# Performance work log

Measured on AMD Instinct MI355X. Metric: run time of the kernel, lower is better.

The kernel has to match this reference:

```python
import jax, jax.numpy as jnp
import numpy as np

N = 1_500_000
NUM_VOXELS = 262_144  # static segment count (replaces torch.unique's dynamic voxel count)
VSIZE = np.array([0.32, 0.32, 0.32], np.float32)
PC_MIN = np.array([-74.88, -74.88, -2.0], np.float32)
GRID = np.array([468, 468, 32], np.int64)
BN_EPS = 1e-3


def setup_inputs() -> dict:
    rng = np.random.default_rng(0)
    # points uniformly inside the point-cloud range -> the range mask is all-true
    xyz = rng.uniform(PC_MIN, PC_MIN + VSIZE * GRID - 1e-3, size=(N, 3)).astype(np.float32)
    feats = rng.uniform(0.0, 1.0, size=(N, 1)).astype(np.float32)
    coords = np.floor((xyz - PC_MIN) / VSIZE).astype(np.int64)
    merge = coords[:, 0] * (GRID[1] * GRID[2]) + coords[:, 1] * GRID[2] + coords[:, 2]
    unq_inv = (merge % NUM_VOXELS).astype(np.int32)  # static-size stand-in for unique inverse ids
    key = jax.random.key(0)
    k1, k2 = jax.random.split(key)
    return {
        'points_xyz': jnp.asarray(xyz),
        'point_feats': jnp.asarray(feats),
        'w1': jax.random.normal(k1, (11, 32), jnp.float32) * 0.1,
        'g1': jnp.ones((32,), jnp.float32),
        'b1': jnp.zeros((32,), jnp.float32),
        'w2': jax.random.normal(k2, (64, 64), jnp.float32) * 0.1,
        'g2': jnp.ones((64,), jnp.float32),
        'b2': jnp.zeros((64,), jnp.float32),
        'unq_inv': jnp.asarray(unq_inv),
    }


def _pfn(x, w, g, b, unq_inv):
    # Linear(bias=False) -> BatchNorm1d(train-mode batch stats, eps=1e-3) -> ReLU -> scatter_max
    y = x @ w
    mu = jnp.mean(y, axis=0)
    var = jnp.var(y, axis=0)
    y = (y - mu) * jax.lax.rsqrt(var + BN_EPS) * g + b
    y = jax.nn.relu(y)
    # relu output >= 0; clamp empty segments (-inf) to 0, matching torch_scatter's zero fill
    y_max = jnp.maximum(jax.ops.segment_max(y, unq_inv, num_segments=NUM_VOXELS), 0.0)
    return y, y_max


def reference(points_xyz, point_feats, w1, g1, b1, w2, g2, b2, unq_inv):
    vsize = jnp.asarray(VSIZE)
    pc_min = jnp.asarray(PC_MIN)
    coords = jnp.floor((points_xyz - pc_min) / vsize)  # [N,3] float voxel coords

    # scatter_mean of xyz per voxel -> cluster-relative offsets
    ones = jnp.ones((points_xyz.shape[0],), points_xyz.dtype)
    cnt = jax.ops.segment_sum(ones, unq_inv, num_segments=NUM_VOXELS)
    vsum = jax.ops.segment_sum(points_xyz, unq_inv, num_segments=NUM_VOXELS)
    vmean = vsum / jnp.maximum(cnt, 1.0)[:, None]
    f_cluster = points_xyz - vmean[unq_inv]

    # offset from voxel center
    f_center = points_xyz - (coords * vsize + vsize * 0.5 + pc_min)
    dist = jnp.linalg.norm(points_xyz, axis=1, keepdims=True)

    feat = jnp.concatenate([points_xyz, point_feats, f_cluster, f_center, dist], axis=-1)  # [N,11]

    x, x_max = _pfn(feat, w1, g1, b1, unq_inv)            # [N,32], [V,32]
    x = jnp.concatenate([x, x_max[unq_inv]], axis=1)       # [N,64]
    _, out = _pfn(x, w2, g2, b2, unq_inv)                  # [V,64] pillar features
    return out
```

## Files before the change

### kernel.cpp

```cpp
#include <hip/hip_runtime.h>

#define NPTS 1500000
#define NVOX 262144
#define BN_EPS 1e-3f
#define PAD 1500160
#define NB_PT 5860
#define NB_L2 11720

typedef __attribute__((ext_vector_type(8))) short bf16x8;
typedef __attribute__((ext_vector_type(4))) float f32x4;

__device__ __forceinline__ unsigned fkey(float f) {
    unsigned u = __float_as_uint(f);
    return u ^ ((unsigned)(((int)u) >> 31) | 0x80000000u);
}
__device__ __forceinline__ float funkey(unsigned k) {
    unsigned u = (k & 0x80000000u) ? (k ^ 0x80000000u) : ~k;
    return __uint_as_float(u);
}
#define KEY_NEG_INF 0x007FFFFFu

__device__ __forceinline__ float bf2f(unsigned short h) {
    union { unsigned u; float f; } x; x.u = ((unsigned)h) << 16; return x.f;
}
__device__ __forceinline__ unsigned short f2bf(float f) {
    union { float f; unsigned u; } x; x.f = f;
    unsigned r = x.u + 0x7FFFu + ((x.u >> 16) & 1u);
    return (unsigned short)(r >> 16);
}
__device__ __forceinline__ unsigned packbf(float a, float b) {
    return (unsigned)f2bf(a) | ((unsigned)f2bf(b) << 16);
}

__device__ __forceinline__ void make_feat(float x, float y, float z, float w,
                                          float mx, float my, float mz, float* f) {
    const float VS = 0.32f;
    const float PMX = -74.88f, PMY = -74.88f, PMZ = -2.0f;
    f[0] = x; f[1] = y; f[2] = z; f[3] = w;
    f[4] = x - mx; f[5] = y - my; f[6] = z - mz;
    float cx = floorf((x - PMX) / VS);
    float cy = floorf((y - PMY) / VS);
    float cz = floorf((z - PMZ) / VS);
    f[7] = x - (cx * VS + 0.5f * VS + PMX);
    f[8] = y - (cy * VS + 0.5f * VS + PMY);
    f[9] = z - (cz * VS + 0.5f * VS + PMZ);
    f[10] = sqrtf(x * x + y * y + z * z);
}

__global__ void k_init(unsigned* __restrict__ okeys, unsigned* __restrict__ xmraw,
                       int* __restrict__ cntv, float* __restrict__ zf,
                       int* __restrict__ svid, const float* __restrict__ w2,
                       uint4* __restrict__ wfrag) {
    long t0 = (long)blockIdx.x * 256 + threadIdx.x;
    long st = (long)gridDim.x * 256;
    uint4 kneg = make_uint4(KEY_NEG_INF, KEY_NEG_INF, KEY_NEG_INF, KEY_NEG_INF);
    for (long i = t0; i < (long)NVOX * 16; i += st) ((uint4*)okeys)[i] = kneg;
    for (long i = t0; i < (long)NVOX * 8; i += st) ((uint4*)xmraw)[i] = kneg;
    for (long i = t0; i < NVOX / 4; i += st) ((int4*)cntv)[i] = make_int4(0, 0, 0, 0);
    for (long i = t0; i < (1024 + 256 * 64 + 256 * 128) / 4; i += st)
        ((float4*)zf)[i] = make_float4(0.f, 0.f, 0.f, 0.f);
    if (t0 < PAD - NPTS) svid[NPTS + t0] = -1;
    if (blockIdx.x == 0 && threadIdx.x < 64) {
        int l = threadIdx.x;
        int lr = l & 15, lk = l >> 4;
        #pragma unroll
        for (int nt = 0; nt < 4; ++nt)
            #pragma unroll
            for (int kt = 0; kt < 2; ++kt) {
                int col = nt * 16 + lr;
                int kb = kt * 32 + lk * 8;
                unsigned u[4];
                #pragma unroll
                for (int j = 0; j < 4; ++j) {
                    float a = w2[(kb + 2 * j) * 64 + col];
                    float b = w2[(kb + 2 * j + 1) * 64 + col];
                    u[j] = packbf(a, b);
                }
                wfrag[(nt * 2 + kt) * 64 + l] = make_uint4(u[0], u[1], u[2], u[3]);
            }
    }
}

__global__ void k_hist(const int* __restrict__ unq, int* __restrict__ cntv) {
    int i = blockIdx.x * blockDim.x + threadIdx.x;
    if (i < NPTS) atomicAdd(&cntv[unq[i]], 1);
}

__global__ void k_scanA(const int* __restrict__ cntv, int* __restrict__ startv,
                        int* __restrict__ bsum) {
    __shared__ int lds[256];
    int t = threadIdx.x;
    int idx4 = blockIdx.x * 256 + t;
    int4 cv = ((const int4*)cntv)[idx4];
    int s0 = cv.x, s1 = s0 + cv.y, s2 = s1 + cv.z, T = s2 + cv.w;
    lds[t] = T;
    __syncthreads();
    for (int o = 1; o < 256; o <<= 1) {
        int v = (t >= o) ? lds[t - o] : 0;
        __syncthreads();
        lds[t] += v;
        __syncthreads();
    }
    int excl = lds[t] - T;
    int4 ov; ov.x = excl; ov.y = excl + s0; ov.z = excl + s1; ov.w = excl + s2;
    ((int4*)startv)[idx4] = ov;
    if (t == 255) bsum[blockIdx.x] = lds[255];
}

__global__ void k_scanC(int* __restrict__ startv, int* __restrict__ offv,
                        const int* __restrict__ bsum) {
    __shared__ int lds[256];
    int t = threadIdx.x;
    int b = bsum[t];
    lds[t] = b;
    __syncthreads();
    for (int o = 1; o < 256; o <<= 1) {
        int v = (t >= o) ? lds[t - o] : 0;
        __syncthreads();
        lds[t] += v;
        __syncthreads();
    }
    int add = (blockIdx.x > 0) ? lds[blockIdx.x - 1] : 0;
    int idx4 = blockIdx.x * 256 + t;
    int4 v = ((int4*)startv)[idx4];
    v.x += add; v.y += add; v.z += add; v.w += add;
    ((int4*)startv)[idx4] = v;
    ((int4*)offv)[idx4] = v;
}

__global__ void k_scatter2(const float* __restrict__ xyz, const float* __restrict__ pf,
                           const int* __restrict__ unq, int* __restrict__ offv,
                           float4* __restrict__ spts, int* __restrict__ svid) {
    int i = blockIdx.x * blockDim.x + threadIdx.x;
    if (i >= NPTS) return;
    int v = unq[i];
    int pos = atomicAdd(&offv[v], 1);
    float4 p;
    p.x = xyz[3 * i + 0]; p.y = xyz[3 * i + 1]; p.z = xyz[3 * i + 2]; p.w = pf[i];
    spts[pos] = p;
    svid[pos] = v;
}

__global__ void k_vmean2(const float4* __restrict__ spts, const int* __restrict__ cntv,
                         const int* __restrict__ startv, float4* __restrict__ vmeanv) {
    int v = blockIdx.x * 256 + threadIdx.x;
    int cnt = cntv[v];
    if (!cnt) return;
    int st = startv[v];
    float sx = 0, sy = 0, sz = 0;
    for (int j = 0; j < cnt; ++j) {
        float4 p = spts[st + j];
        sx += p.x; sy += p.y; sz += p.z;
    }
    float inv = 1.0f / (float)cnt;
    vmeanv[v] = make_float4(sx * inv, sy * inv, sz * inv, 0.f);
}

__device__ __forceinline__ void flush32(int v, float m, bool atom, int c,
                                        unsigned* __restrict__ xm) {
    if ((unsigned)v >= (unsigned)NVOX) return;
    if (atom) atomicMax(&xm[(size_t)v * 32 + c], fkey(m));
    else xm[(size_t)v * 32 + c] = fkey(m);
}
__device__ __forceinline__ void flush64(int v, float m, bool atom, int c,
                                        unsigned* __restrict__ ok) {
    if ((unsigned)v >= (unsigned)NVOX) return;
    if (atom) atomicMax(&ok[(size_t)v * 64 + c], fkey(m));
    else ok[(size_t)v * 64 + c] = fkey(m);
}

__global__ __launch_bounds__(256) void k_passA(
    const float4* __restrict__ spts, const int* __restrict__ svid,
    const float4* __restrict__ vmeanv, const float* __restrict__ w1,
    unsigned* __restrict__ xmraw, unsigned* __restrict__ y1bf,
    float* __restrict__ spart1) {
    __shared__ float ylds[4][32 * 33];
    int t = threadIdx.x;
    int lane = t & 63, wave = t >> 6;
    int rl = lane & 31, half = lane >> 5;
    long grow = (long)blockIdx.x * 128 + wave * 32 + rl;
    int vid = svid[grow];
    float yv[16];
    #pragma unroll
    for (int j = 0; j < 16; ++j) yv[j] = 0.f;
    if (vid >= 0) {
        float4 p = spts[grow];
        float4 vm = vmeanv[vid];
        float f[11];
        make_feat(p.x, p.y, p.z, p.w, vm.x, vm.y, vm.z, f);
        const float4* w1f = (const float4*)w1;
        #pragma unroll
        for (int k = 0; k < 11; ++k) {
            float fk = f[k];
            #pragma unroll
            for (int q = 0; q < 4; ++q) {
                float4 wq = w1f[k * 8 + half * 4 + q];
                yv[4 * q + 0] = fmaf(fk, wq.x, yv[4 * q + 0]);
                yv[4 * q + 1] = fmaf(fk, wq.y, yv[4 * q + 1]);
                yv[4 * q + 2] = fmaf(fk, wq.z, yv[4 * q + 2]);
                yv[4 * q + 3] = fmaf(fk, wq.w, yv[4 * q + 3]);
            }
        }
    }
    {
        unsigned ypk[8];
        #pragma unroll
        for (int q = 0; q < 8; ++q) ypk[q] = packbf(yv[2 * q], yv[2 * q + 1]);
        uint4* yb = (uint4*)y1bf;
        yb[grow * 4 + half * 2 + 0] = *(const uint4*)&ypk[0];
        yb[grow * 4 + half * 2 + 1] = *(const uint4*)&ypk[4];
    }
    float* yw = &ylds[wave][0];
    #pragma unroll
    for (int j = 0; j < 16; ++j) yw[rl * 33 + half * 16 + j] = yv[j];
    asm volatile("s_waitcnt lgkmcnt(0)" ::: "memory");
    __builtin_amdgcn_sched_barrier(0);
    int c = rl;
    int r0 = half * 16;
    float sa = 0.f, sq = 0.f;
    int cur_v = -2; float cur_m = 0.f; bool first = true;
    #pragma unroll
    for (int i = 0; i < 16; ++i) {
        int r = r0 + i;
        float y = yw[r * 33 + c];
        int v = __shfl(vid, r);
        sa += y; sq += y * y;
        if (i == 0) { cur_v = v; cur_m = y; }
        else if (v == cur_v) cur_m = fmaxf(cur_m, y);
        else {
            flush32(cur_v, cur_m, first, c, xmraw);
            first = false; cur_v = v; cur_m = y;
        }
    }
    flush32(cur_v, cur_m, true, c, xmraw);
    sa += __shfl_xor(sa, 32);
    sq += __shfl_xor(sq, 32);
    if (half == 0) {
        int slot = (blockIdx.x * 4 + wave) & 255;
        atomicAdd(&spart1[slot * 64 + c], sa);
        atomicAdd(&spart1[slot * 64 + 32 + c], sq);
    }
}

__global__ void k_fin1(const float* __restrict__ spart1, float* __restrict__ stats,
                       const float* __restrict__ g1, const float* __restrict__ b1) {
    __shared__ float cs[64];
    int t = threadIdx.x;
    float s = 0.f;
    for (int r = 0; r < 256; ++r) s += spart1[r * 64 + t];
    cs[t] = s;
    __syncthreads();
    if (t < 32) {
        float invn = 1.0f / (float)NPTS;
        float mu = cs[t] * invn;
        float var = cs[32 + t] * invn - mu * mu;
        float sc = rsqrtf(var + BN_EPS) * g1[t];
        stats[64 + t] = sc;
        stats[96 + t] = b1[t] - mu * sc;
    }
}

__global__ void k_xmz(const unsigned* __restrict__ xmraw,
                      const float* __restrict__ stats, unsigned* __restrict__ zxm) {
    int tid = blockIdx.x * 256 + threadIdx.x;
    int v = tid >> 2, q = tid & 3;
    uint4 a = ((const uint4*)xmraw)[v * 8 + q * 2];
    uint4 b = ((const uint4*)xmraw)[v * 8 + q * 2 + 1];
    float4 sc0 = ((const float4*)(stats + 64))[q * 2];
    float4 sh0 = ((const float4*)(stats + 96))[q * 2];
    float4 sc1 = ((const float4*)(stats + 64))[q * 2 + 1];
    float4 sh1 = ((const float4*)(stats + 96))[q * 2 + 1];
    uint4 o;
    o.x = packbf(fmaxf(0.f, fmaf(funkey(a.x), sc0.x, sh0.x)),
                 fmaxf(0.f, fmaf(funkey(a.y), sc0.y, sh0.y)));
    o.y = packbf(fmaxf(0.f, fmaf(funkey(a.z), sc0.z, sh0.z)),
                 fmaxf(0.f, fmaf(funkey(a.w), sc0.w, sh0.w)));
    o.z = packbf(fmaxf(0.f, fmaf(funkey(b.x), sc1.x, sh1.x)),
                 fmaxf(0.f, fmaf(funkey(b.y), sc1.y, sh1.y)));
    o.w = packbf(fmaxf(0.f, fmaf(funkey(b.z), sc1.z, sh1.z)),
                 fmaxf(0.f, fmaf(funkey(b.w), sc1.w, sh1.w)));
    ((uint4*)zxm)[v * 4 + q] = o;
}

__global__ __launch_bounds__(256) void k_l2(
    const int* __restrict__ svid, const unsigned* __restrict__ y1bf,
    const unsigned* __restrict__ zxm, const uint4* __restrict__ wfrag,
    const float* __restrict__ stats, float* __restrict__ spart2,
    unsigned* __restrict__ okeys) {
    __shared__ unsigned shbuf[4][1088];
    int t = threadIdx.x;
    int lane = t & 63, wave = t >> 6;
    int rl = lane & 31, half = lane >> 5;
    int lr = lane & 15, lk = lane >> 4;
    long brow = (long)blockIdx.x * 128 + wave * 32;
    int vid = svid[brow + rl];
    int vprev = __shfl(vid, (lane + 63) & 63);
    unsigned mask32 = (unsigned)(__ballot(rl > 0 && vid != vprev) & 0xFFFFFFFFull);

    uint4 bw[8];
    #pragma unroll
    for (int q = 0; q < 8; ++q) bw[q] = wfrag[q * 64 + lane];
    uint4 yu0 = ((const uint4*)y1bf)[(brow + rl) * 4 + half * 2];
    uint4 yu1 = ((const uint4*)y1bf)[(brow + rl) * 4 + half * 2 + 1];
    uint4 xa = make_uint4(0, 0, 0, 0), xb = make_uint4(0, 0, 0, 0);
    if (vid >= 0) {
        xa = ((const uint4*)zxm)[(size_t)vid * 4 + half * 2];
        xb = ((const uint4*)zxm)[(size_t)vid * 4 + half * 2 + 1];
    }

    unsigned zpk[8];
    if (vid >= 0) {
        unsigned yw[8] = {yu0.x, yu0.y, yu0.z, yu0.w, yu1.x, yu1.y, yu1.z, yu1.w};
        #pragma unroll
        for (int q = 0; q < 4; ++q) {
            float4 sc = ((const float4*)(stats + 64))[half * 4 + q];
            float4 sh = ((const float4*)(stats + 96))[half * 4 + q];
            float yA = bf2f((unsigned short)(yw[2 * q] & 0xFFFF));
            float yB = bf2f((unsigned short)(yw[2 * q] >> 16));
            float yC = bf2f((unsigned short)(yw[2 * q + 1] & 0xFFFF));
            float yD = bf2f((unsigned short)(yw[2 * q + 1] >> 16));
            zpk[2 * q + 0] = packbf(fmaxf(0.f, fmaf(yA, sc.x, sh.x)),
                                    fmaxf(0.f, fmaf(yB, sc.y, sh.y)));
            zpk[2 * q + 1] = packbf(fmaxf(0.f, fmaf(yC, sc.z, sh.z)),
                                    fmaxf(0.f, fmaf(yD, sc.w, sh.w)));
        }
    } else {
        #pragma unroll
        for (int q = 0; q < 8; ++q) zpk[q] = 0u;
    }
    {
        uint4* arow = (uint4*)&shbuf[wave][rl * 32];
        int sw = rl & 7;
        arow[(2 * half + 0) ^ sw] = *(const uint4*)&zpk[0];
        arow[(2 * half + 1) ^ sw] = *(const uint4*)&zpk[4];
        arow[(4 + 2 * half) ^ sw] = xa;
        arow[(5 + 2 * half) ^ sw] = xb;
    }
    asm volatile("s_waitcnt lgkmcnt(0)" ::: "memory");
    __builtin_amdgcn_sched_barrier(0);

    bf16x8 afr[2][2];
    #pragma unroll
    for (int mt = 0; mt < 2; ++mt)
        #pragma unroll
        for (int kt = 0; kt < 2; ++kt) {
            int riw = mt * 16 + lr;
            uint4 uu = ((const uint4*)&shbuf[wave][riw * 32])[(kt * 4 + lk) ^ (riw & 7)];
            afr[mt][kt] = __builtin_bit_cast(bf16x8, uu);
        }
    asm volatile("s_waitcnt lgkmcnt(0)" ::: "memory");
    __builtin_amdgcn_sched_barrier(0);

    f32x4 acc[2][4];
    #pragma unroll
    for (int mt = 0; mt < 2; ++mt)
        #pragma unroll
        for (int nt = 0; nt < 4; ++nt) {
            acc[mt][nt] = (f32x4){0.f, 0.f, 0.f, 0.f};
            #pragma unroll
            for (int kt = 0; kt < 2; ++kt)
                acc[mt][nt] = __builtin_amdgcn_mfma_f32_16x16x32_bf16(
                    afr[mt][kt], __builtin_bit_cast(bf16x8, bw[nt * 2 + kt]),
                    acc[mt][nt], 0, 0, 0);
        }

    unsigned* y2w = &shbuf[wave][0];
    #pragma unroll
    for (int mt = 0; mt < 2; ++mt)
        #pragma unroll
        for (int nt = 0; nt < 4; ++nt) {
            int col = nt * 16 + lr;
            int w0 = mt * 8 + lk * 2;
            y2w[col * 17 + w0] = packbf(acc[mt][nt][0], acc[mt][nt][1]);
            y2w[col * 17 + w0 + 1] = packbf(acc[mt][nt][2], acc[mt][nt][3]);
        }

    {
        float sa[4] = {0.f, 0.f, 0.f, 0.f}, sq[4] = {0.f, 0.f, 0.f, 0.f};
        #pragma unroll
        for (int mt = 0; mt < 2; ++mt)
            #pragma unroll
            for (int nt = 0; nt < 4; ++nt)
                #pragma unroll
                for (int e = 0; e < 4; ++e) {
                    float v = acc[mt][nt][e];
                    sa[nt] += v; sq[nt] += v * v;
                }
        #pragma unroll
        for (int nt = 0; nt < 4; ++nt) {
            sa[nt] += __shfl_xor(sa[nt], 16); sa[nt] += __shfl_xor(sa[nt], 32);
            sq[nt] += __shfl_xor(sq[nt], 16); sq[nt] += __shfl_xor(sq[nt], 32);
        }
        if (lk == 0) {
            int slot = (blockIdx.x * 4 + wave) & 255;
            #pragma unroll
            for (int nt = 0; nt < 4; ++nt) {
                atomicAdd(&spart2[slot * 128 + nt * 16 + lr], sa[nt]);
                atomicAdd(&spart2[slot * 128 + 64 + nt * 16 + lr], sq[nt]);
            }
        }
    }
    asm volatile("s_waitcnt lgkmcnt(0)" ::: "memory");
    __builtin_amdgcn_sched_barrier(0);

    {
        int c = lane;
        float cur_m = 0.f; bool first = true;
        #pragma unroll
        for (int q = 0; q < 16; ++q) {
            unsigned u = y2w[c * 17 + q];
            #pragma unroll
            for (int e = 0; e < 2; ++e) {
                int r = 2 * q + e;
                float d = bf2f((unsigned short)(e ? (u >> 16) : (u & 0xFFFF)));
                if (r == 0) cur_m = d;
                else if ((mask32 >> r) & 1u) {
                    int v = __shfl(vid, r - 1);
                    flush64(v, cur_m, first, c, okeys);
                    first = false; cur_m = d;
                } else cur_m = fmaxf(cur_m, d);
            }
        }
        int vlast = __shfl(vid, 31);
        flush64(vlast, cur_m, true, c, okeys);
    }
}

__global__ void k_fin2(const float* __restrict__ spart2, float* __restrict__ stats,
                       const float* __restrict__ g2, const float* __restrict__ b2) {
    __shared__ float cs[128];
    int t = threadIdx.x;
    float s = 0.f;
    for (int r = 0; r < 256; ++r) s += spart2[r * 128 + t];
    cs[t] = s;
    __syncthreads();
    if (t < 64) {
        float invn = 1.0f / (float)NPTS;
        float mu = cs[t] * invn;
        float var = cs[64 + t] * invn - mu * mu;
        float sc = rsqrtf(var + BN_EPS) * g2[t];
        stats[256 + t] = sc;
        stats[320 + t] = b2[t] - mu * sc;
    }
}

__global__ void k_out(unsigned* __restrict__ okeys, const float* __restrict__ stats) {
    int i4 = blockIdx.x * 256 + threadIdx.x;
    uint4 u = ((const uint4*)okeys)[i4];
    int c0 = (i4 & 15) * 4;
    float4 o;
    o.x = fmaxf(0.f, fmaf(funkey(u.x), stats[256 + c0 + 0], stats[320 + c0 + 0]));
    o.y = fmaxf(0.f, fmaf(funkey(u.y), stats[256 + c0 + 1], stats[320 + c0 + 1]));
    o.z = fmaxf(0.f, fmaf(funkey(u.z), stats[256 + c0 + 2], stats[320 + c0 + 2]));
    o.w = fmaxf(0.f, fmaf(funkey(u.w), stats[256 + c0 + 3], stats[320 + c0 + 3]));
    ((float4*)okeys)[i4] = o;
}

extern "C" void kernel_launch(void* const* d_in, const int* in_sizes, int n_in,
                              void* d_out, int out_size, void* d_ws, size_t ws_size,
                              hipStream_t stream) {
    const float* xyz = (const float*)d_in[0];
    const float* pf  = (const float*)d_in[1];
    const float* w1  = (const float*)d_in[2];
    const float* g1  = (const float*)d_in[3];
    const float* b1  = (const float*)d_in[4];
    const float* w2  = (const float*)d_in[5];
    const float* g2  = (const float*)d_in[6];
    const float* b2  = (const float*)d_in[7];
    const int*   unq = (const int*)d_in[8];

    float4* spts     = (float4*)d_ws;
    float4* vmeanv   = spts + PAD;
    int* svid        = (int*)(vmeanv + NVOX);
    unsigned* xmraw  = (unsigned*)(svid + PAD);
    int* cntv        = (int*)(xmraw + (size_t)NVOX * 32);
    int* startv      = cntv + NVOX;
    int* offv        = startv + NVOX;
    int* bsum        = offv + NVOX;
    float* stats     = (float*)(bsum + 256);
    float* spart1    = stats + 1024;
    float* spart2    = spart1 + 256 * 64;
    uint4* wfrag     = (uint4*)(spart2 + 256 * 128);
    unsigned* y1bf   = (unsigned*)(wfrag + 512);
    unsigned* zxm    = (unsigned*)spts;

    unsigned* okeys = (unsigned*)d_out;

    k_init<<<2048, 256, 0, stream>>>(okeys, xmraw, cntv, stats, svid, w2, wfrag);
    k_hist<<<NB_PT, 256, 0, stream>>>(unq, cntv);
    k_scanA<<<256, 256, 0, stream>>>(cntv, startv, bsum);
    k_scanC<<<256, 256, 0, stream>>>(startv, offv, bsum);
    k_scatter2<<<NB_PT, 256, 0, stream>>>(xyz, pf, unq, offv, spts, svid);
    k_vmean2<<<NVOX / 256, 256, 0, stream>>>(spts, cntv, startv, vmeanv);
    k_passA<<<NB_L2, 256, 0, stream>>>(spts, svid, vmeanv, w1, xmraw, y1bf, spart1);
    k_fin1<<<1, 64, 0, stream>>>(spart1, stats, g1, b1);
    k_xmz<<<NVOX * 4 / 256, 256, 0, stream>>>(xmraw, stats, zxm);
    k_l2<<<NB_L2, 256, 0, stream>>>(svid, y1bf, zxm, wfrag, stats, spart2, okeys);
    k_fin2<<<1, 128, 0, stream>>>(spart2, stats, g2, b2);
    k_out<<<NVOX * 16 / 256, 256, 0, stream>>>(okeys, stats);
}
```

Before: 378.1 us.

## Replace per-voxel atomic scatter with two-level bucket scatter and local sort

Points are first scattered into 2048 coarse buckets of 128 voxels using one global atomic counter per bucket, written to a staging buffer that reuses the y1bf space. A per-bucket kernel then places points at their final voxel positions using LDS atomics. The aim is to make the global writes and atomics in the scatter more localized and coalesced. The cost is an extra pass over the staged data, and the bucket counters become heavily contended global atomics.

```diff
diff --git a/kernel.cpp b/kernel.cpp
--- a/kernel.cpp
+++ b/kernel.cpp
@@ -6,6 +6,7 @@
 #define PAD 1500160
 #define NB_PT 5860
 #define NB_L2 11720
+#define NBUK 2048
 
 typedef __attribute__((ext_vector_type(8))) short bf16x8;
 typedef __attribute__((ext_vector_type(4))) float f32x4;
@@ -107,7 +108,7 @@
     if (t == 255) bsum[blockIdx.x] = lds[255];
 }
 
-__global__ void k_scanC(int* __restrict__ startv, int* __restrict__ offv,
+__global__ void k_scanC(int* __restrict__ startv, int* __restrict__ bukcur,
                         const int* __restrict__ bsum) {
     __shared__ int lds[256];
     int t = threadIdx.x;
@@ -125,20 +126,42 @@
     int4 v = ((int4*)startv)[idx4];
     v.x += add; v.y += add; v.z += add; v.w += add;
     ((int4*)startv)[idx4] = v;
-    ((int4*)offv)[idx4] = v;
-}
-
-__global__ void k_scatter2(const float* __restrict__ xyz, const float* __restrict__ pf,
-                           const int* __restrict__ unq, int* __restrict__ offv,
-                           float4* __restrict__ spts, int* __restrict__ svid) {
+    int vox0 = idx4 * 4;
+    if ((vox0 & 127) == 0) bukcur[vox0 >> 7] = v.x;
+}
+
+__global__ void k_bscat(const float* __restrict__ xyz, const float* __restrict__ pf,
+                        const int* __restrict__ unq, int* __restrict__ bukcur,
+                        float4* __restrict__ stage_p, int* __restrict__ stage_v) {
     int i = blockIdx.x * blockDim.x + threadIdx.x;
     if (i >= NPTS) return;
     int v = unq[i];
-    int pos = atomicAdd(&offv[v], 1);
+    int pos = atomicAdd(&bukcur[v >> 7], 1);
     float4 p;
     p.x = xyz[3 * i + 0]; p.y = xyz[3 * i + 1]; p.z = xyz[3 * i + 2]; p.w = pf[i];
-    spts[pos] = p;
-    svid[pos] = v;
+    stage_p[pos] = p;
+    stage_v[pos] = v;
+}
+
+__global__ __launch_bounds__(256) void k_bsort(
+    const float4* __restrict__ stage_p, const int* __restrict__ stage_v,
+    const int* __restrict__ startv, float4* __restrict__ spts,
+    int* __restrict__ svid) {
+    __shared__ int cnt[128];
+    int t = threadIdx.x;
+    if (t < 128) cnt[t] = 0;
+    __syncthreads();
+    int b = blockIdx.x;
+    int bstart = startv[b << 7];
+    int bend = (b == NBUK - 1) ? NPTS : startv[(b + 1) << 7];
+    for (int j = bstart + t; j < bend; j += 256) {
+        float4 p = stage_p[j];
+        int v = stage_v[j];
+        int lr = atomicAdd(&cnt[v & 127], 1);
+        int pos = startv[v] + lr;
+        spts[pos] = p;
+        svid[pos] = v;
+    }
 }
 
 __global__ void k_vmean2(const float4* __restrict__ spts, const int* __restrict__ cntv,
@@ -475,13 +498,15 @@
     unsigned* xmraw  = (unsigned*)(svid + PAD);
     int* cntv        = (int*)(xmraw + (size_t)NVOX * 32);
     int* startv      = cntv + NVOX;
-    int* offv        = startv + NVOX;
-    int* bsum        = offv + NVOX;
+    int* bukcur      = startv + NVOX;
+    int* bsum        = bukcur + NVOX;
     float* stats     = (float*)(bsum + 256);
     float* spart1    = stats + 1024;
     float* spart2    = spart1 + 256 * 64;
     uint4* wfrag     = (uint4*)(spart2 + 256 * 128);
     unsigned* y1bf   = (unsigned*)(wfrag + 512);
+    float4* stage_p  = (float4*)y1bf;
+    int* stage_v     = (int*)(stage_p + PAD);
     unsigned* zxm    = (unsigned*)spts;
 
     unsigned* okeys = (unsigned*)d_out;
@@ -489,8 +514,9 @@
     k_init<<<2048, 256, 0, stream>>>(okeys, xmraw, cntv, stats, svid, w2, wfrag);
     k_hist<<<NB_PT, 256, 0, stream>>>(unq, cntv);
     k_scanA<<<256, 256, 0, stream>>>(cntv, startv, bsum);
-    k_scanC<<<256, 256, 0, stream>>>(startv, offv, bsum);
-    k_scatter2<<<NB_PT, 256, 0, stream>>>(xyz, pf, unq, offv, spts, svid);
+    k_scanC<<<256, 256, 0, stream>>>(startv, bukcur, bsum);
+    k_bscat<<<NB_PT, 256, 0, stream>>>(xyz, pf, unq, bukcur, stage_p, stage_v);
+    k_bsort<<<NBUK, 256, 0, stream>>>(stage_p, stage_v, startv, spts, svid);
     k_vmean2<<<NVOX / 256, 256, 0, stream>>>(spts, cntv, startv, vmeanv);
     k_passA<<<NB_L2, 256, 0, stream>>>(spts, svid, vmeanv, w1, xmraw, y1bf, spart1);
     k_fin1<<<1, 64, 0, stream>>>(spart1, stats, g1, b1);
```

After: 482.5 us. 27.6% more time.

## Scatter point indices instead of point payloads and gather lazily

Applied to the files above, without the earlier changes.

The sort-by-voxel step now writes only a 4-byte source index per point instead of a float4 payload plus voxel id. Voxel ids are filled in a separate per-voxel kernel, and the mean and first-layer kernels gather xyz and features through the index. This cuts scattered write traffic but adds an extra kernel and replaces coalesced float4 reads with indirect, uncoalesced gathers from the original arrays. The workspace layout changes, and zxm gets its own buffer instead of aliasing spts.

```diff
diff --git a/kernel.cpp b/kernel.cpp
--- a/kernel.cpp
+++ b/kernel.cpp
@@ -128,29 +128,34 @@
     ((int4*)offv)[idx4] = v;
 }
 
-__global__ void k_scatter2(const float* __restrict__ xyz, const float* __restrict__ pf,
-                           const int* __restrict__ unq, int* __restrict__ offv,
-                           float4* __restrict__ spts, int* __restrict__ svid) {
+__global__ void k_scatteridx(const int* __restrict__ unq, int* __restrict__ offv,
+                             int* __restrict__ sidx) {
     int i = blockIdx.x * blockDim.x + threadIdx.x;
     if (i >= NPTS) return;
     int v = unq[i];
     int pos = atomicAdd(&offv[v], 1);
-    float4 p;
-    p.x = xyz[3 * i + 0]; p.y = xyz[3 * i + 1]; p.z = xyz[3 * i + 2]; p.w = pf[i];
-    spts[pos] = p;
-    svid[pos] = v;
-}
-
-__global__ void k_vmean2(const float4* __restrict__ spts, const int* __restrict__ cntv,
-                         const int* __restrict__ startv, float4* __restrict__ vmeanv) {
+    sidx[pos] = i;
+}
+
+__global__ void k_fillvid(const int* __restrict__ cntv, const int* __restrict__ startv,
+                          int* __restrict__ svid) {
+    int v = blockIdx.x * 256 + threadIdx.x;
+    int cnt = cntv[v];
+    int st = startv[v];
+    for (int j = 0; j < cnt; ++j) svid[st + j] = v;
+}
+
+__global__ void k_vmean2(const float* __restrict__ xyz, const int* __restrict__ sidx,
+                         const int* __restrict__ cntv, const int* __restrict__ startv,
+                         float4* __restrict__ vmeanv) {
     int v = blockIdx.x * 256 + threadIdx.x;
     int cnt = cntv[v];
     if (!cnt) return;
     int st = startv[v];
     float sx = 0, sy = 0, sz = 0;
     for (int j = 0; j < cnt; ++j) {
-        float4 p = spts[st + j];
-        sx += p.x; sy += p.y; sz += p.z;
+        int idx = sidx[st + j];
+        sx += xyz[3 * idx + 0]; sy += xyz[3 * idx + 1]; sz += xyz[3 * idx + 2];
     }
     float inv = 1.0f / (float)cnt;
     vmeanv[v] = make_float4(sx * inv, sy * inv, sz * inv, 0.f);
@@ -170,7 +175,8 @@
 }
 
 __global__ __launch_bounds__(256) void k_passA(
-    const float4* __restrict__ spts, const int* __restrict__ svid,
+    const float* __restrict__ xyz, const float* __restrict__ pf,
+    const int* __restrict__ sidx, const int* __restrict__ svid,
     const float4* __restrict__ vmeanv, const float* __restrict__ w1,
     unsigned* __restrict__ xmraw, unsigned* __restrict__ y1bf,
     float* __restrict__ spart1) {
@@ -184,10 +190,12 @@
     #pragma unroll
     for (int j = 0; j < 16; ++j) yv[j] = 0.f;
     if (vid >= 0) {
-        float4 p = spts[grow];
+        int idx = sidx[grow];
+        float px = xyz[3 * idx + 0], py = xyz[3 * idx + 1], pz = xyz[3 * idx + 2];
+        float pw = pf[idx];
         float4 vm = vmeanv[vid];
         float f[11];
-        make_feat(p.x, p.y, p.z, p.w, vm.x, vm.y, vm.z, f);
+        make_feat(px, py, pz, pw, vm.x, vm.y, vm.z, f);
         const float4* w1f = (const float4*)w1;
         #pragma unroll
         for (int k = 0; k < 11; ++k) {
@@ -469,11 +477,12 @@
     const float* b2  = (const float*)d_in[7];
     const int*   unq = (const int*)d_in[8];
 
-    float4* spts     = (float4*)d_ws;
-    float4* vmeanv   = spts + PAD;
-    int* svid        = (int*)(vmeanv + NVOX);
-    unsigned* xmraw  = (unsigned*)(svid + PAD);
-    int* cntv        = (int*)(xmraw + (size_t)NVOX * 32);
+    int* sidx        = (int*)d_ws;
+    int* svid        = sidx + PAD;
+    float4* vmeanv   = (float4*)(svid + PAD);
+    unsigned* xmraw  = (unsigned*)(vmeanv + NVOX);
+    unsigned* zxm    = xmraw + (size_t)NVOX * 32;
+    int* cntv        = (int*)(zxm + (size_t)NVOX * 16);
     int* startv      = cntv + NVOX;
     int* offv        = startv + NVOX;
     int* bsum        = offv + NVOX;
@@ -482,7 +491,6 @@
     float* spart2    = spart1 + 256 * 64;
     uint4* wfrag     = (uint4*)(spart2 + 256 * 128);
     unsigned* y1bf   = (unsigned*)(wfrag + 512);
-    unsigned* zxm    = (unsigned*)spts;
 
     unsigned* okeys = (unsigned*)d_out;
 
@@ -490,9 +498,11 @@
     k_hist<<<NB_PT, 256, 0, stream>>>(unq, cntv);
     k_scanA<<<256, 256, 0, stream>>>(cntv, startv, bsum);
     k_scanC<<<256, 256, 0, stream>>>(startv, offv, bsum);
-    k_scatter2<<<NB_PT, 256, 0, stream>>>(xyz, pf, unq, offv, spts, svid);
-    k_vmean2<<<NVOX / 256, 256, 0, stream>>>(spts, cntv, startv, vmeanv);
-    k_passA<<<NB_L2, 256, 0, stream>>>(spts, svid, vmeanv, w1, xmraw, y1bf, spart1);
+    k_scatteridx<<<NB_PT, 256, 0, stream>>>(unq, offv, sidx);
+    k_fillvid<<<NVOX / 256, 256, 0, stream>>>(cntv, startv, svid);
+    k_vmean2<<<NVOX / 256, 256, 0, stream>>>(xyz, sidx, cntv, startv, vmeanv);
+    k_passA<<<NB_L2, 256, 0, stream>>>(xyz, pf, sidx, svid, vmeanv, w1, xmraw,
+                                       y1bf, spart1);
     k_fin1<<<1, 64, 0, stream>>>(spart1, stats, g1, b1);
     k_xmz<<<NVOX * 4 / 256, 256, 0, stream>>>(xmraw, stats, zxm);
     k_l2<<<NB_L2, 256, 0, stream>>>(svid, y1bf, zxm, wfrag, stats, spart2, okeys);
```

After: 434.1 us. 14.8% more time.
